# Kernel optimization log

Measured on AMD Instinct MI355X. Metric: run time of the kernel, lower is better.

The kernel has to match this reference:

```python
import jax, jax.numpy as jnp
import numpy as np

D_MODEL = 64

def setup_inputs() -> dict:
    key = jax.random.key(0)
    k1, k2, k3, k4 = jax.random.split(key, 4)
    B, T, E = 4, 4096, 128
    x = jax.random.normal(k1, (B, T, E), dtype=jnp.float32)
    # nn.Linear weights, stored transposed as (in, out) for x @ W
    s = 1.0 / np.sqrt(E)
    Wq = jax.random.uniform(k2, (E, D_MODEL), jnp.float32, -s, s)
    Wk = jax.random.uniform(k3, (E, D_MODEL), jnp.float32, -s, s)
    Wv = jax.random.uniform(k4, (E, D_MODEL), jnp.float32, -s, s)
    return {"x": x, "Wq": Wq, "Wk": Wk, "Wv": Wv}

def reference(x, Wq, Wk, Wv):
    B, T, E = x.shape
    q = jnp.einsum('bte,ed->btd', x, Wq)
    k = jnp.einsum('bte,ed->btd', x, Wk)
    v = jnp.einsum('bte,ed->btd', x, Wv)
    scores = jnp.einsum('bqd,bkd->bqk', q, k) / np.sqrt(D_MODEL)  # [B,T,T]
    causal = jnp.tril(jnp.ones((T, T), dtype=bool))
    scores = jnp.where(causal, scores, jnp.float32(-1e9))
    attn = jax.nn.softmax(scores, axis=-1)
    # dropout p=0.0 -> identity (eval-mode faithful)
    return jnp.einsum('bqk,bkd->bqd', attn, v)
```

## Files before the change

kernel.cpp:

```cpp
#include <hip/hip_runtime.h>
#include <hip/hip_bf16.h>


typedef __attribute__((ext_vector_type(4))) float  f32x4;
typedef __attribute__((ext_vector_type(4))) unsigned int u32x4;
typedef __attribute__((ext_vector_type(8))) __bf16 bf16x8;
typedef __attribute__((ext_vector_type(8))) unsigned short u16x8;
typedef __attribute__((ext_vector_type(4))) unsigned short u16x4;

#define T_SEQ 4096
#define DH    64
#define EDIM  128
#define KVB   64
#define KSTR  72
#define VSTR  136
#define QSCALE 0.18033688f

__device__ __forceinline__ unsigned short f2bf(float f) {
    unsigned int x = __builtin_bit_cast(unsigned int, f);
    unsigned int r = x + 0x7fffu + ((x >> 16) & 1u);
    return (unsigned short)(r >> 16);
}

__device__ __forceinline__ unsigned int cvt_pk_bf16(float lo, float hi) {
    unsigned int d;
    asm("v_cvt_pk_bf16_f32 %0, %1, %2" : "=v"(d) : "v"(lo), "v"(hi));
    return d;
}

__device__ __forceinline__ f32x4 mfma_bf16(u16x8 a, u16x8 b, f32x4 c) {
    return __builtin_amdgcn_mfma_f32_16x16x32_bf16(
        __builtin_bit_cast(bf16x8, a), __builtin_bit_cast(bf16x8, b), c, 0, 0, 0);
}

__global__ __launch_bounds__(256) void prep_w_kernel(
    const float* __restrict__ wq, const float* __restrict__ wk,
    const float* __restrict__ wv, unsigned short* __restrict__ wt)
{
    int o = blockIdx.x * 256 + threadIdx.x;
    int m   = o >> 13;
    int rem = o & 8191;
    int d = rem >> 7, e = rem & 127;
    const float* W = (m == 0) ? wq : (m == 1) ? wk : wv;
    wt[o] = f2bf(W[e * DH + d]);
}

__global__ __launch_bounds__(64) void proj_kernel(
    const float* __restrict__ x, const unsigned short* __restrict__ wt,
    unsigned short* __restrict__ qw, unsigned short* __restrict__ kw,
    unsigned short* __restrict__ vt)
{
    const int l   = threadIdx.x;
    const int l15 = l & 15;
    const int lg  = l >> 4;
    const int row0 = blockIdx.x * 16;
    const int b    = row0 >> 12;
    const int t0   = row0 & 4095;

    u16x8 af[4];
    #pragma unroll
    for (int kt = 0; kt < 4; ++kt) {
        const float* xp = x + (row0 + l15) * EDIM + kt * 32 + lg * 8;
        f32x4 a = *(const f32x4*)xp;
        f32x4 bb = *(const f32x4*)(xp + 4);
        af[kt] = u16x8{ f2bf(a[0]), f2bf(a[1]), f2bf(a[2]), f2bf(a[3]),
                        f2bf(bb[0]), f2bf(bb[1]), f2bf(bb[2]), f2bf(bb[3]) };
    }

    unsigned short* outs[2] = { qw, kw };
    #pragma unroll
    for (int m = 0; m < 2; ++m) {
        #pragma unroll
        for (int nt = 0; nt < 4; ++nt) {
            f32x4 acc = {};
            #pragma unroll
            for (int kt = 0; kt < 4; ++kt) {
                u16x8 bfrag = *(const u16x8*)(wt + (m * 64 + nt * 16 + l15) * EDIM
                                                 + kt * 32 + lg * 8);
                acc = mfma_bf16(af[kt], bfrag, acc);
            }
            const float sc = (m == 0) ? QSCALE : 1.0f;
            #pragma unroll
            for (int r = 0; r < 4; ++r)
                outs[m][(row0 + lg * 4 + r) * DH + nt * 16 + l15] = f2bf(acc[r] * sc);
        }
    }

    #pragma unroll
    for (int nt = 0; nt < 4; ++nt) {
        f32x4 acc = {};
        #pragma unroll
        for (int kt = 0; kt < 4; ++kt) {
            u16x8 bfrag = *(const u16x8*)(wt + (2 * 64 + nt * 16 + l15) * EDIM
                                             + kt * 32 + lg * 8);
            acc = mfma_bf16(af[kt], bfrag, acc);
        }
        u16x4 pv = { f2bf(acc[0]), f2bf(acc[1]), f2bf(acc[2]), f2bf(acc[3]) };
        *(u16x4*)(vt + ((size_t)(b * DH + nt * 16 + l15)) * T_SEQ + t0 + lg * 4) = pv;
    }
}

__device__ __forceinline__ void loadK(u16x8 kr[4], const unsigned short* kgB,
                                      int kv0, int tid) {
    #pragma unroll
    for (int j = 0; j < 4; ++j) {
        int gi = tid + j * 256;
        kr[j] = *(const u16x8*)(kgB + (size_t)(kv0 + (gi >> 3)) * DH + (gi & 7) * 8);
    }
}
__device__ __forceinline__ void loadV(u16x8 vr[4], const unsigned short* vtB,
                                      int kv0, int tid) {
    #pragma unroll
    for (int j = 0; j < 4; ++j) {
        int gi = tid + j * 256;
        vr[j] = *(const u16x8*)(vtB + (size_t)(gi >> 4) * T_SEQ + kv0 + (gi & 15) * 8);
    }
}
__device__ __forceinline__ void writeK(const u16x8 kr[4], unsigned short* K_lds,
                                       int tid) {
    #pragma unroll
    for (int j = 0; j < 4; ++j) {
        int gi = tid + j * 256;
        *(u16x8*)&K_lds[(gi >> 3) * KSTR + (gi & 7) * 8] = kr[j];
    }
}
__device__ __forceinline__ void writeV(const u16x8 vr[4], unsigned short* V_lds,
                                       int tid) {
    #pragma unroll
    for (int j = 0; j < 4; ++j) {
        int gi = tid + j * 256;
        *(u16x8*)&V_lds[(gi >> 4) * VSTR + (gi & 15) * 8] = vr[j];
    }
}

__global__ __launch_bounds__(256, 3) void attn_partial_kernel(
    const unsigned short* __restrict__ qg, const unsigned short* __restrict__ kg,
    const unsigned short* __restrict__ vt,
    unsigned short* __restrict__ po, float* __restrict__ pm, float* __restrict__ pl)
{
    const int bid = blockIdx.x;
    const int b   = bid / 272;
    const int i   = bid - b * 272;
    int k = (int)((__builtin_sqrtf((float)(4 * i + 1)) - 1.0f) * 0.5f);
    while (k * (k + 1) > i) --k;
    while ((k + 1) * (k + 2) <= i) ++k;
    const int r    = i - k * (k + 1);
    const int hiq  = (r >= k + 1);
    const int q128 = 2 * k + hiq;
    const int ch   = hiq ? r - (k + 1) : r;

    __shared__ unsigned short K_lds[128 * KSTR];
    __shared__ unsigned short V_lds[64 * VSTR];

    const int tid = threadIdx.x;
    const int w   = tid >> 6;
    const int l   = tid & 63;
    const int l15 = l & 15;
    const int lg  = l >> 4;

    const int base   = b * T_SEQ;
    const int qrow0w = q128 * 128 + w * 32;
    const int kvb = ch * 256;
    const int kve = min(kvb + 256, q128 * 128 + 128);
    const bool ng2 = (kve - kvb) > 128;

    const unsigned short* kgB = kg + (size_t)base * DH;
    const unsigned short* vtB = vt + (size_t)b * DH * T_SEQ;

    u16x8 qf[2][2];
    #pragma unroll
    for (int rt = 0; rt < 2; ++rt) {
        const unsigned short* qrow = qg + (base + qrow0w + rt * 16 + l15) * DH;
        qf[rt][0] = *(const u16x8*)(qrow + 0 + lg * 8);
        qf[rt][1] = *(const u16x8*)(qrow + 32 + lg * 8);
    }

    f32x4 o_acc[2][4];
    float m_run[2], l_run[2];
    #pragma unroll
    for (int rt = 0; rt < 2; ++rt) {
        #pragma unroll
        for (int dt = 0; dt < 4; ++dt) o_acc[rt][dt] = f32x4{};
        m_run[rt] = -1e30f; l_run[rt] = 0.0f;
    }

    const int src0 = l15 + 32 * (lg & 1);
    const int src1 = src0 + 16;
    const bool hi  = (lg >> 1) != 0;

    auto compute_tile = [&](int kv0, int tt) {
        if (kv0 > qrow0w + 31) return;
        const unsigned short* Kt = K_lds + (tt * 64) * KSTR;
        const unsigned short* Vt = V_lds + tt * 64;

        u16x8 kf[4][2];
        #pragma unroll
        for (int nt = 0; nt < 4; ++nt)
            #pragma unroll
            for (int kt = 0; kt < 2; ++kt)
                kf[nt][kt] = *(const u16x8*)&Kt[(nt * 16 + l15) * KSTR
                                                + kt * 32 + lg * 8];

        f32x4 s[2][4];
        __builtin_amdgcn_s_setprio(1);
        #pragma unroll
        for (int rt = 0; rt < 2; ++rt)
            #pragma unroll
            for (int nt = 0; nt < 4; ++nt) {
                f32x4 a = {};
                a = mfma_bf16(kf[nt][0], qf[rt][0], a);
                a = mfma_bf16(kf[nt][1], qf[rt][1], a);
                s[rt][nt] = a;
            }
        __builtin_amdgcn_s_setprio(0);

        if (kv0 + KVB - 1 > qrow0w) {
            #pragma unroll
            for (int rt = 0; rt < 2; ++rt)
                #pragma unroll
                for (int nt = 0; nt < 4; ++nt)
                    #pragma unroll
                    for (int rr = 0; rr < 4; ++rr) {
                        int kj = kv0 + nt * 16 + lg * 4 + rr;
                        int qi = qrow0w + rt * 16 + l15;
                        if (kj > qi) s[rt][nt][rr] = -1e30f;
                    }
        }

        float sc2[2];
        bool grow = false;
        unsigned int pk[2][4][2];
        #pragma unroll
        for (int rt = 0; rt < 2; ++rt) {
            float mx = s[rt][0][0];
            #pragma unroll
            for (int nt = 0; nt < 4; ++nt)
                #pragma unroll
                for (int rr = 0; rr < 4; ++rr)
                    mx = fmaxf(mx, s[rt][nt][rr]);
            mx = fmaxf(mx, __shfl_xor(mx, 16));
            mx = fmaxf(mx, __shfl_xor(mx, 32));

            float mold = m_run[rt];
            float mnew = fmaxf(mold, mx);
            grow |= (mx > mold);
            float sc = exp2f(mold - mnew);
            sc2[rt] = sc;
            m_run[rt] = mnew;

            float rs = 0.0f;
            #pragma unroll
            for (int nt = 0; nt < 4; ++nt)
                #pragma unroll
                for (int rr = 0; rr < 4; ++rr) {
                    float p = exp2f(s[rt][nt][rr] - mnew);
                    s[rt][nt][rr] = p;
                    rs += p;
                }
            rs += __shfl_xor(rs, 16);
            rs += __shfl_xor(rs, 32);
            l_run[rt] = l_run[rt] * sc + rs;

            #pragma unroll
            for (int nt = 0; nt < 4; ++nt) {
                pk[rt][nt][0] = cvt_pk_bf16(s[rt][nt][0], s[rt][nt][1]);
                pk[rt][nt][1] = cvt_pk_bf16(s[rt][nt][2], s[rt][nt][3]);
            }
        }
        if (__any(grow)) {
            #pragma unroll
            for (int rt = 0; rt < 2; ++rt)
                #pragma unroll
                for (int dt = 0; dt < 4; ++dt)
                    o_acc[rt][dt] *= sc2[rt];
        }

        __builtin_amdgcn_s_setprio(1);
        #pragma unroll
        for (int kt = 0; kt < 2; ++kt) {
            u16x8 vf[4];
            #pragma unroll
            for (int dt = 0; dt < 4; ++dt)
                vf[dt] = *(const u16x8*)&Vt[(dt * 16 + l15) * VSTR
                                            + kt * 32 + lg * 8];
            #pragma unroll
            for (int rt = 0; rt < 2; ++rt) {
                unsigned int pb[4];
                #pragma unroll
                for (int t = 0; t < 4; ++t) {
                    int src = (t < 2) ? src0 : src1;
                    unsigned int pa  = __shfl(pk[rt][2 * kt][t & 1], src);
                    unsigned int pbv = __shfl(pk[rt][2 * kt + 1][t & 1], src);
                    pb[t] = hi ? pbv : pa;
                }
                u32x4 pbq = { pb[0], pb[1], pb[2], pb[3] };
                u16x8 pbf = __builtin_bit_cast(u16x8, pbq);
                #pragma unroll
                for (int dt = 0; dt < 4; ++dt)
                    o_acc[rt][dt] = mfma_bf16(vf[dt], pbf, o_acc[rt][dt]);
            }
        }
        __builtin_amdgcn_s_setprio(0);
    };

    u16x8 kr[4], vr[4];
    loadK(kr, kgB, kvb, tid);
    loadV(vr, vtB, kvb, tid);
    writeK(kr, K_lds, tid);
    writeV(vr, V_lds, tid);
    __syncthreads();

    if (ng2) loadK(kr, kgB, kvb + 128, tid);
    compute_tile(kvb, 0);
    if (ng2) loadV(vr, vtB, kvb + 128, tid);
    compute_tile(kvb + 64, 1);
    __syncthreads();

    if (ng2) {
        writeK(kr, K_lds, tid);
        writeV(vr, V_lds, tid);
        __syncthreads();
        compute_tile(kvb + 128, 0);
        compute_tile(kvb + 192, 1);
    }

    const int pidx = (b * 32 + q128) * 16 + ch;
    unsigned short* pob = po + (size_t)pidx * 8192;
    #pragma unroll
    for (int rt = 0; rt < 2; ++rt) {
        int row = w * 32 + rt * 16 + l15;
        #pragma unroll
        for (int dt = 0; dt < 4; ++dt) {
            unsigned int w0 = cvt_pk_bf16(o_acc[rt][dt][0], o_acc[rt][dt][1]);
            unsigned int w1 = cvt_pk_bf16(o_acc[rt][dt][2], o_acc[rt][dt][3]);
            *(unsigned int*)&pob[row * 64 + dt * 16 + lg * 4]     = w0;
            *(unsigned int*)&pob[row * 64 + dt * 16 + lg * 4 + 2] = w1;
        }
        if (lg == 0) {
            pm[pidx * 128 + row] = m_run[rt];
            pl[pidx * 128 + row] = l_run[rt];
        }
    }
}

__global__ __launch_bounds__(256) void attn_combine_kernel(
    const unsigned short* __restrict__ po, const float* __restrict__ pm,
    const float* __restrict__ pl, float* __restrict__ out)
{
    const int blk  = blockIdx.x;
    const int half = blk & 1;
    const int tb   = blk >> 1;
    const int q128 = tb & 31;
    const int b    = tb >> 5;
    const int nch  = (q128 >> 1) + 1;
    const int row  = half * 64 + (threadIdx.x >> 2);
    const int d0   = (threadIdx.x & 3) * 16;
    const int bp   = tb * 16;

    float mstar = -1e30f;
    for (int i = 0; i < nch; ++i)
        mstar = fmaxf(mstar, pm[(bp + i) * 128 + row]);

    float lsum = 0.0f;
    float a[16] = {};
    for (int i = 0; i < nch; ++i) {
        float wi = exp2f(pm[(bp + i) * 128 + row] - mstar);
        lsum += wi * pl[(bp + i) * 128 + row];
        const unsigned short* p = po + (size_t)(bp + i) * 8192 + row * 64 + d0;
        u16x8 v0 = *(const u16x8*)p;
        u16x8 v1 = *(const u16x8*)(p + 8);
        #pragma unroll
        for (int j = 0; j < 8; ++j) {
            unsigned int u0 = (unsigned int)v0[j] << 16;
            unsigned int u1 = (unsigned int)v1[j] << 16;
            a[j]     += wi * __builtin_bit_cast(float, u0);
            a[8 + j] += wi * __builtin_bit_cast(float, u1);
        }
    }
    const float inv = 1.0f / lsum;
    float* op = out + (size_t)(b * T_SEQ + q128 * 128 + row) * DH + d0;
    #pragma unroll
    for (int j = 0; j < 4; ++j) {
        f32x4 o0 = { a[4*(j&1)+0 + 8*(j>>1)] * inv, a[4*(j&1)+1 + 8*(j>>1)] * inv,
                     a[4*(j&1)+2 + 8*(j>>1)] * inv, a[4*(j&1)+3 + 8*(j>>1)] * inv };
        *(f32x4*)(op + j * 4) = o0;
    }
}

__global__ __launch_bounds__(64, 4) void attn_direct_kernel(
    const unsigned short* __restrict__ qg, const unsigned short* __restrict__ kg,
    const unsigned short* __restrict__ vt, float* __restrict__ out)
{
    const int bid = blockIdx.x;
    const int q32 = bid & 127;
    const int b   = bid >> 7;
    const int l = threadIdx.x, l15 = l & 15, lg = l >> 4;
    const int qrow0 = q32 * 32;
    const int base  = b * T_SEQ;
    const unsigned short* kp = kg + (size_t)base * DH;
    const unsigned short* vp = vt + (size_t)b * DH * T_SEQ;

    u16x8 qf[2][2];
    #pragma unroll
    for (int rt = 0; rt < 2; ++rt) {
        const unsigned short* qrow = qg + (base + qrow0 + rt * 16 + l15) * DH;
        qf[rt][0] = *(const u16x8*)(qrow + 0 + lg * 8);
        qf[rt][1] = *(const u16x8*)(qrow + 32 + lg * 8);
    }

    f32x4 o_acc[2][4];
    float m_run[2], l_run[2];
    #pragma unroll
    for (int rt = 0; rt < 2; ++rt) {
        #pragma unroll
        for (int dt = 0; dt < 4; ++dt) o_acc[rt][dt] = f32x4{};
        m_run[rt] = -1e30f; l_run[rt] = 0.0f;
    }

    const int src0 = l15 + 32 * (lg & 1);
    const int src1 = src0 + 16;
    const bool hi  = (lg >> 1) != 0;

    for (int kv0 = 0; kv0 <= qrow0 + 31; kv0 += KVB) {
        u16x8 kf[4][2];
        #pragma unroll
        for (int nt = 0; nt < 4; ++nt)
            #pragma unroll
            for (int kt = 0; kt < 2; ++kt)
                kf[nt][kt] = *(const u16x8*)(kp + (kv0 + nt * 16 + l15) * DH
                                                + kt * 32 + lg * 8);
        f32x4 s[2][4];
        #pragma unroll
        for (int rt = 0; rt < 2; ++rt)
            #pragma unroll
            for (int nt = 0; nt < 4; ++nt) {
                f32x4 a = {};
                a = mfma_bf16(kf[nt][0], qf[rt][0], a);
                a = mfma_bf16(kf[nt][1], qf[rt][1], a);
                s[rt][nt] = a;
            }
        if (kv0 + KVB - 1 > qrow0) {
            #pragma unroll
            for (int rt = 0; rt < 2; ++rt)
                #pragma unroll
                for (int nt = 0; nt < 4; ++nt)
                    #pragma unroll
                    for (int rr = 0; rr < 4; ++rr) {
                        int kj = kv0 + nt * 16 + lg * 4 + rr;
                        int qi = qrow0 + rt * 16 + l15;
                        if (kj > qi) s[rt][nt][rr] = -1e30f;
                    }
        }
        float sc2[2];
        bool grow = false;
        unsigned int pk[2][4][2];
        #pragma unroll
        for (int rt = 0; rt < 2; ++rt) {
            float mx = s[rt][0][0];
            #pragma unroll
            for (int nt = 0; nt < 4; ++nt)
                #pragma unroll
                for (int rr = 0; rr < 4; ++rr)
                    mx = fmaxf(mx, s[rt][nt][rr]);
            mx = fmaxf(mx, __shfl_xor(mx, 16));
            mx = fmaxf(mx, __shfl_xor(mx, 32));
            float mold = m_run[rt];
            float mnew = fmaxf(mold, mx);
            grow |= (mx > mold);
            float sc = exp2f(mold - mnew);
            sc2[rt] = sc;
            m_run[rt] = mnew;
            float rs = 0.0f;
            #pragma unroll
            for (int nt = 0; nt < 4; ++nt)
                #pragma unroll
                for (int rr = 0; rr < 4; ++rr) {
                    float p = exp2f(s[rt][nt][rr] - mnew);
                    s[rt][nt][rr] = p;
                    rs += p;
                }
            rs += __shfl_xor(rs, 16);
            rs += __shfl_xor(rs, 32);
            l_run[rt] = l_run[rt] * sc + rs;
            #pragma unroll
            for (int nt = 0; nt < 4; ++nt) {
                pk[rt][nt][0] = cvt_pk_bf16(s[rt][nt][0], s[rt][nt][1]);
                pk[rt][nt][1] = cvt_pk_bf16(s[rt][nt][2], s[rt][nt][3]);
            }
        }
        if (__any(grow)) {
            #pragma unroll
            for (int rt = 0; rt < 2; ++rt)
                #pragma unroll
                for (int dt = 0; dt < 4; ++dt)
                    o_acc[rt][dt] *= sc2[rt];
        }
        #pragma unroll
        for (int kt = 0; kt < 2; ++kt) {
            u16x8 vf[4];
            #pragma unroll
            for (int dt = 0; dt < 4; ++dt)
                vf[dt] = *(const u16x8*)(vp + (size_t)(dt * 16 + l15) * T_SEQ
                                            + kv0 + kt * 32 + lg * 8);
            #pragma unroll
            for (int rt = 0; rt < 2; ++rt) {
                unsigned int pb[4];
                #pragma unroll
                for (int t = 0; t < 4; ++t) {
                    int src = (t < 2) ? src0 : src1;
                    unsigned int pa  = __shfl(pk[rt][2 * kt][t & 1], src);
                    unsigned int pbv = __shfl(pk[rt][2 * kt + 1][t & 1], src);
                    pb[t] = hi ? pbv : pa;
                }
                u32x4 pbq = { pb[0], pb[1], pb[2], pb[3] };
                u16x8 pbf = __builtin_bit_cast(u16x8, pbq);
                #pragma unroll
                for (int dt = 0; dt < 4; ++dt)
                    o_acc[rt][dt] = mfma_bf16(vf[dt], pbf, o_acc[rt][dt]);
            }
        }
    }

    #pragma unroll
    for (int rt = 0; rt < 2; ++rt) {
        float inv = 1.0f / l_run[rt];
        int row = base + qrow0 + rt * 16 + l15;
        #pragma unroll
        for (int dt = 0; dt < 4; ++dt) {
            f32x4 ov = o_acc[rt][dt] * inv;
            *(f32x4*)&out[(size_t)row * DH + dt * 16 + lg * 4] = ov;
        }
    }
}

extern "C" void kernel_launch(void* const* d_in, const int* in_sizes, int n_in,
                              void* d_out, int out_size, void* d_ws, size_t ws_size,
                              hipStream_t stream)
{
    const float* x  = (const float*)d_in[0];
    const float* wq = (const float*)d_in[1];
    const float* wk = (const float*)d_in[2];
    const float* wv = (const float*)d_in[3];
    float* out = (float*)d_out;

    unsigned short* wt = (unsigned short*)d_ws;
    unsigned short* qw = (unsigned short*)((char*)d_ws + 65536);
    unsigned short* kw = qw + (size_t)16384 * DH;
    unsigned short* vt = kw + (size_t)16384 * DH;

    const size_t po_off = 65536u + 3u * 16384u * DH * 2u;
    const size_t po_sz  = (size_t)2048 * 128 * 64 * 2;
    const size_t pm_off = po_off + po_sz;
    const size_t pl_off = pm_off + (size_t)2048 * 128 * 4;
    const size_t need   = pl_off + (size_t)2048 * 128 * 4;

    prep_w_kernel<<<96, 256, 0, stream>>>(wq, wk, wv, wt);
    proj_kernel<<<1024, 64, 0, stream>>>(x, wt, qw, kw, vt);

    if (ws_size >= need) {
        unsigned short* po = (unsigned short*)((char*)d_ws + po_off);
        float* pm = (float*)((char*)d_ws + pm_off);
        float* pl = (float*)((char*)d_ws + pl_off);
        attn_partial_kernel<<<4 * 272, 256, 0, stream>>>(qw, kw, vt, po, pm, pl);
        attn_combine_kernel<<<4 * 32 * 2, 256, 0, stream>>>(po, pm, pl, out);
    } else {
        attn_direct_kernel<<<4 * 128, 64, 0, stream>>>(qw, kw, vt, out);
    }
}
```

Before: 60.53 us.

## Split attention into 128-key chunks per block with finer combine

Each partial-attention block now covers one 128-wide KV chunk instead of up to 256, giving 528 triangular work items per batch instead of 272. The in-block two-stage register prefetch of the second KV half is dropped, and the launch bound asks for 4 blocks per CU. The aim is finer parallelism and better load balance across CUs. The combine kernel is reworked to 4 row slices with 8 columns per thread, so it now merges up to 32 partials per row. The cost is more partial-output writes and combine reads, plus the loss of load/compute overlap inside a block.

Result: slower. 63.91 us (+5.6%).

```diff
diff --git a/kernel.cpp b/kernel.cpp
--- a/kernel.cpp
+++ b/kernel.cpp
@@ -15,6 +15,7 @@
 #define KSTR  72
 #define VSTR  136
 #define QSCALE 0.18033688f
+#define NTRI  528
 
 __device__ __forceinline__ unsigned short f2bf(float f) {
     unsigned int x = __builtin_bit_cast(unsigned int, f);
@@ -100,54 +101,19 @@
     }
 }
 
-__device__ __forceinline__ void loadK(u16x8 kr[4], const unsigned short* kgB,
-                                      int kv0, int tid) {
-    #pragma unroll
-    for (int j = 0; j < 4; ++j) {
-        int gi = tid + j * 256;
-        kr[j] = *(const u16x8*)(kgB + (size_t)(kv0 + (gi >> 3)) * DH + (gi & 7) * 8);
-    }
-}
-__device__ __forceinline__ void loadV(u16x8 vr[4], const unsigned short* vtB,
-                                      int kv0, int tid) {
-    #pragma unroll
-    for (int j = 0; j < 4; ++j) {
-        int gi = tid + j * 256;
-        vr[j] = *(const u16x8*)(vtB + (size_t)(gi >> 4) * T_SEQ + kv0 + (gi & 15) * 8);
-    }
-}
-__device__ __forceinline__ void writeK(const u16x8 kr[4], unsigned short* K_lds,
-                                       int tid) {
-    #pragma unroll
-    for (int j = 0; j < 4; ++j) {
-        int gi = tid + j * 256;
-        *(u16x8*)&K_lds[(gi >> 3) * KSTR + (gi & 7) * 8] = kr[j];
-    }
-}
-__device__ __forceinline__ void writeV(const u16x8 vr[4], unsigned short* V_lds,
-                                       int tid) {
-    #pragma unroll
-    for (int j = 0; j < 4; ++j) {
-        int gi = tid + j * 256;
-        *(u16x8*)&V_lds[(gi >> 4) * VSTR + (gi & 15) * 8] = vr[j];
-    }
-}
-
-__global__ __launch_bounds__(256, 3) void attn_partial_kernel(
+__global__ __launch_bounds__(256, 4) void attn_partial_kernel(
     const unsigned short* __restrict__ qg, const unsigned short* __restrict__ kg,
     const unsigned short* __restrict__ vt,
     unsigned short* __restrict__ po, float* __restrict__ pm, float* __restrict__ pl)
 {
     const int bid = blockIdx.x;
-    const int b   = bid / 272;
-    const int i   = bid - b * 272;
-    int k = (int)((__builtin_sqrtf((float)(4 * i + 1)) - 1.0f) * 0.5f);
-    while (k * (k + 1) > i) --k;
-    while ((k + 1) * (k + 2) <= i) ++k;
-    const int r    = i - k * (k + 1);
-    const int hiq  = (r >= k + 1);
-    const int q128 = 2 * k + hiq;
-    const int ch   = hiq ? r - (k + 1) : r;
+    const int b   = bid / NTRI;
+    const int i   = bid - b * NTRI;
+    int q = (int)((__builtin_sqrtf((float)(8 * i + 1)) - 1.0f) * 0.5f);
+    while (q * (q + 1) / 2 > i) --q;
+    while ((q + 1) * (q + 2) / 2 <= i) ++q;
+    const int q128 = q;
+    const int ch   = i - q * (q + 1) / 2;
 
     __shared__ unsigned short K_lds[128 * KSTR];
     __shared__ unsigned short V_lds[64 * VSTR];
@@ -160,12 +126,26 @@
 
     const int base   = b * T_SEQ;
     const int qrow0w = q128 * 128 + w * 32;
-    const int kvb = ch * 256;
-    const int kve = min(kvb + 256, q128 * 128 + 128);
-    const bool ng2 = (kve - kvb) > 128;
+    const int kvb    = ch * 128;
 
     const unsigned short* kgB = kg + (size_t)base * DH;
     const unsigned short* vtB = vt + (size_t)b * DH * T_SEQ;
+
+    {
+        u16x8 kr[4], vr[4];
+        #pragma unroll
+        for (int j = 0; j < 4; ++j) {
+            int gi = tid + j * 256;
+            kr[j] = *(const u16x8*)(kgB + (size_t)(kvb + (gi >> 3)) * DH + (gi & 7) * 8);
+            vr[j] = *(const u16x8*)(vtB + (size_t)(gi >> 4) * T_SEQ + kvb + (gi & 15) * 8);
+        }
+        #pragma unroll
+        for (int j = 0; j < 4; ++j) {
+            int gi = tid + j * 256;
+            *(u16x8*)&K_lds[(gi >> 3) * KSTR + (gi & 7) * 8] = kr[j];
+            *(u16x8*)&V_lds[(gi >> 4) * VSTR + (gi & 15) * 8] = vr[j];
+        }
+    }
 
     u16x8 qf[2][2];
     #pragma unroll
@@ -188,8 +168,12 @@
     const int src1 = src0 + 16;
     const bool hi  = (lg >> 1) != 0;
 
-    auto compute_tile = [&](int kv0, int tt) {
-        if (kv0 > qrow0w + 31) return;
+    __syncthreads();
+
+    #pragma unroll
+    for (int tt = 0; tt < 2; ++tt) {
+        const int kv0 = kvb + tt * 64;
+        if (kv0 > qrow0w + 31) continue;
         const unsigned short* Kt = K_lds + (tt * 64) * KSTR;
         const unsigned short* Vt = V_lds + tt * 64;
 
@@ -301,30 +285,9 @@
             }
         }
         __builtin_amdgcn_s_setprio(0);
-    };
-
-    u16x8 kr[4], vr[4];
-    loadK(kr, kgB, kvb, tid);
-    loadV(vr, vtB, kvb, tid);
-    writeK(kr, K_lds, tid);
-    writeV(vr, V_lds, tid);
-    __syncthreads();
-
-    if (ng2) loadK(kr, kgB, kvb + 128, tid);
-    compute_tile(kvb, 0);
-    if (ng2) loadV(vr, vtB, kvb + 128, tid);
-    compute_tile(kvb + 64, 1);
-    __syncthreads();
-
-    if (ng2) {
-        writeK(kr, K_lds, tid);
-        writeV(vr, V_lds, tid);
-        __syncthreads();
-        compute_tile(kvb + 128, 0);
-        compute_tile(kvb + 192, 1);
-    }
-
-    const int pidx = (b * 32 + q128) * 16 + ch;
+    }
+
+    const int pidx = bid;
     unsigned short* pob = po + (size_t)pidx * 8192;
     #pragma unroll
     for (int rt = 0; rt < 2; ++rt) {
@@ -347,44 +310,38 @@
     const unsigned short* __restrict__ po, const float* __restrict__ pm,
     const float* __restrict__ pl, float* __restrict__ out)
 {
-    const int blk  = blockIdx.x;
-    const int half = blk & 1;
-    const int tb   = blk >> 1;
-    const int q128 = tb & 31;
-    const int b    = tb >> 5;
-    const int nch  = (q128 >> 1) + 1;
-    const int row  = half * 64 + (threadIdx.x >> 2);
-    const int d0   = (threadIdx.x & 3) * 16;
-    const int bp   = tb * 16;
+    const int blk   = blockIdx.x;
+    const int slice = blk & 3;
+    const int tb    = blk >> 2;
+    const int q128  = tb & 31;
+    const int b     = tb >> 5;
+    const int nch   = q128 + 1;
+    const int bslot = b * NTRI + q128 * (q128 + 1) / 2;
+    const int row   = slice * 32 + (threadIdx.x >> 3);
+    const int d0    = (threadIdx.x & 7) * 8;
 
     float mstar = -1e30f;
     for (int i = 0; i < nch; ++i)
-        mstar = fmaxf(mstar, pm[(bp + i) * 128 + row]);
+        mstar = fmaxf(mstar, pm[(bslot + i) * 128 + row]);
 
     float lsum = 0.0f;
-    float a[16] = {};
+    float a[8] = {};
     for (int i = 0; i < nch; ++i) {
-        float wi = exp2f(pm[(bp + i) * 128 + row] - mstar);
-        lsum += wi * pl[(bp + i) * 128 + row];
-        const unsigned short* p = po + (size_t)(bp + i) * 8192 + row * 64 + d0;
-        u16x8 v0 = *(const u16x8*)p;
-        u16x8 v1 = *(const u16x8*)(p + 8);
+        float wi = exp2f(pm[(bslot + i) * 128 + row] - mstar);
+        lsum += wi * pl[(bslot + i) * 128 + row];
+        u16x8 v = *(const u16x8*)&po[(size_t)(bslot + i) * 8192 + row * 64 + d0];
         #pragma unroll
         for (int j = 0; j < 8; ++j) {
-            unsigned int u0 = (unsigned int)v0[j] << 16;
-            unsigned int u1 = (unsigned int)v1[j] << 16;
-            a[j]     += wi * __builtin_bit_cast(float, u0);
-            a[8 + j] += wi * __builtin_bit_cast(float, u1);
+            unsigned int u = (unsigned int)v[j] << 16;
+            a[j] += wi * __builtin_bit_cast(float, u);
         }
     }
     const float inv = 1.0f / lsum;
     float* op = out + (size_t)(b * T_SEQ + q128 * 128 + row) * DH + d0;
-    #pragma unroll
-    for (int j = 0; j < 4; ++j) {
-        f32x4 o0 = { a[4*(j&1)+0 + 8*(j>>1)] * inv, a[4*(j&1)+1 + 8*(j>>1)] * inv,
-                     a[4*(j&1)+2 + 8*(j>>1)] * inv, a[4*(j&1)+3 + 8*(j>>1)] * inv };
-        *(f32x4*)(op + j * 4) = o0;
-    }
+    f32x4 o0 = { a[0] * inv, a[1] * inv, a[2] * inv, a[3] * inv };
+    f32x4 o1 = { a[4] * inv, a[5] * inv, a[6] * inv, a[7] * inv };
+    *(f32x4*)op = o0;
+    *(f32x4*)(op + 4) = o1;
 }
 
 __global__ __launch_bounds__(64, 4) void attn_direct_kernel(
@@ -548,11 +505,12 @@
     unsigned short* kw = qw + (size_t)16384 * DH;
     unsigned short* vt = kw + (size_t)16384 * DH;
 
+    const size_t slots  = 4u * NTRI;
     const size_t po_off = 65536u + 3u * 16384u * DH * 2u;
-    const size_t po_sz  = (size_t)2048 * 128 * 64 * 2;
+    const size_t po_sz  = slots * 8192 * 2;
     const size_t pm_off = po_off + po_sz;
-    const size_t pl_off = pm_off + (size_t)2048 * 128 * 4;
-    const size_t need   = pl_off + (size_t)2048 * 128 * 4;
+    const size_t pl_off = pm_off + slots * 128 * 4;
+    const size_t need   = pl_off + slots * 128 * 4;
 
     prep_w_kernel<<<96, 256, 0, stream>>>(wq, wk, wv, wt);
     proj_kernel<<<1024, 64, 0, stream>>>(x, wt, qw, kw, vt);
@@ -561,8 +519,8 @@
         unsigned short* po = (unsigned short*)((char*)d_ws + po_off);
         float* pm = (float*)((char*)d_ws + pm_off);
         float* pl = (float*)((char*)d_ws + pl_off);
-        attn_partial_kernel<<<4 * 272, 256, 0, stream>>>(qw, kw, vt, po, pm, pl);
-        attn_combine_kernel<<<4 * 32 * 2, 256, 0, stream>>>(po, pm, pl, out);
+        attn_partial_kernel<<<4 * NTRI, 256, 0, stream>>>(qw, kw, vt, po, pm, pl);
+        attn_combine_kernel<<<4 * 32 * 4, 256, 0, stream>>>(po, pm, pl, out);
     } else {
         attn_direct_kernel<<<4 * 128, 64, 0, stream>>>(qw, kw, vt, out);
     }
```
